# Optimization experiments

Hardware: AMD Instinct MI355X
Metric: run time of the kernel (lower is better)

Reference implementation:

```python
import jax, jax.numpy as jnp
import numpy as np

IN_DIM = 784
HIDDEN = 512
STYLE = 128
BATCH = 2048
NUM_LABELS = 10


def setup_inputs() -> dict:
    key = jax.random.key(0)
    k1, k2, k3, k4 = jax.random.split(key, 4)
    x = jax.random.uniform(k1, (BATCH, IN_DIM), dtype=jnp.float32)
    m = jax.random.randint(k2, (BATCH,), 0, NUM_LABELS)
    # Embedding tables, scaled as in the torch __init__ (N(0,1)/fan)
    fc1_table = jax.random.normal(k3, (NUM_LABELS, (IN_DIM + 1) * HIDDEN), dtype=jnp.float32) / ((IN_DIM + 1) * HIDDEN)
    fc2_table = jax.random.normal(k4, (NUM_LABELS, (HIDDEN + 1) * STYLE), dtype=jnp.float32) / ((HIDDEN + 1) * STYLE)
    return {"x": x, "m": m, "fc1_table": fc1_table, "fc2_table": fc2_table}


def reference(x, m, fc1_table, fc2_table):
    B = x.shape[0]
    x = x.reshape(B, -1)  # [B, 784]
    # Per-sample weight matrices gathered by label
    fc1 = fc1_table[m].reshape(B, IN_DIM + 1, HIDDEN)   # [B, 785, H]
    fc1_w, fc1_b = fc1[:, :IN_DIM, :], fc1[:, -1, :]
    h1 = jax.nn.relu(jnp.einsum('bkj,bk->bj', fc1_w, x) + fc1_b)  # [B, H]
    fc2 = fc2_table[m].reshape(B, HIDDEN + 1, STYLE)    # [B, H+1, S]
    fc2_w, fc2_b = fc2[:, :HIDDEN, :], fc2[:, -1, :]
    h2 = jnp.einsum('bkj,bk->bj', fc2_w, h1) + fc2_b    # [B, S]
    return jax.nn.sigmoid(h2)
```

## Files before the change

kernel.cpp:

```cpp
#include <hip/hip_runtime.h>
#include <hip/hip_bf16.h>
#include <math.h>

#define BATCH      2048
#define IN_DIM     784
#define HIDDEN     512
#define STYLE      128
#define NUM_LABELS 10
#define FC1_STRIDE ((IN_DIM + 1) * HIDDEN)
#define FC2_STRIDE ((HIDDEN + 1) * STYLE)
#define KP1        832
#define TB         64
#define BK         64
#define MAX_TILES  48

#define META_NTILES 31
#define META_TILES  32
#define META_PERM   176

#define W1B_OFF  16384ULL
#define W2B_OFF  (W1B_OFF + 10ULL*HIDDEN*KP1*2)
#define H1B_OFF  (W2B_OFF + 10ULL*STYLE*HIDDEN*2)
#define BF16_NEED (H1B_OFF + (size_t)BATCH*HIDDEN*2)

#define W1_KB 26
#define W1_NB 16
#define W2_KB 16
#define W2_NB 4
#define W1_BLOCKS (W1_KB*W1_NB*NUM_LABELS)
#define W2_BLOCKS (W2_KB*W2_NB*NUM_LABELS)

typedef short short8  __attribute__((ext_vector_type(8)));
typedef float float4e __attribute__((ext_vector_type(4)));

__device__ __forceinline__ ushort f2b(float v) {
    __hip_bfloat16 h = __float2bfloat16(v);
    return *reinterpret_cast<ushort*>(&h);
}

__global__ void k_prep(const int* __restrict__ m, const float* __restrict__ fc1t,
                       const float* __restrict__ fc2t, int* __restrict__ meta,
                       ushort* __restrict__ w1b, ushort* __restrict__ w2b) {
    const int tid = threadIdx.x;
    int bid = blockIdx.x;

    __shared__ int cnt[NUM_LABELS], curs[NUM_LABELS], offs[NUM_LABELS + 1];
    __shared__ int permS[BATCH];
    __shared__ float tile[32][33];

    if (bid == 0) {
        if (tid < NUM_LABELS) { cnt[tid] = 0; curs[tid] = 0; }
        __syncthreads();
        for (int b = tid; b < BATCH; b += 256) atomicAdd(&cnt[m[b]], 1);
        __syncthreads();
        if (tid == 0) {
            int off = 0;
            for (int L = 0; L < NUM_LABELS; ++L) { offs[L] = off; off += cnt[L]; }
            offs[NUM_LABELS] = off;
        }
        __syncthreads();
        for (int b = tid; b < BATCH; b += 256) {
            int L = m[b];
            int r = atomicAdd(&curs[L], 1);
            permS[offs[L] + r] = b;
        }
        __syncthreads();
        for (int i = tid; i < BATCH; i += 256) meta[META_PERM + i] = permS[i];
        if (tid == 0) {
            int idx = 0;
            for (int L = 0; L < NUM_LABELS; ++L) {
                int c = cnt[L], off = offs[L];
                for (int t = 0; t < c; t += TB) {
                    meta[META_TILES + idx * 3 + 0] = L;
                    meta[META_TILES + idx * 3 + 1] = off + t;
                    meta[META_TILES + idx * 3 + 2] = min(TB, c - t);
                    ++idx;
                }
            }
            meta[META_NTILES] = idx;
        }
        return;
    }

    bid -= 1;
    const float* src; ushort* dst; int Kvalid, Kpad, N, kb, nb, L; size_t srcL, dstL;
    if (bid < W1_BLOCKS) {
        kb = bid % W1_KB; nb = (bid / W1_KB) % W1_NB; L = bid / (W1_KB * W1_NB);
        src = fc1t; dst = w1b; Kvalid = IN_DIM; Kpad = KP1; N = HIDDEN;
        srcL = FC1_STRIDE; dstL = (size_t)HIDDEN * KP1;
    } else {
        bid -= W1_BLOCKS;
        kb = bid % W2_KB; nb = (bid / W2_KB) % W2_NB; L = bid / (W2_KB * W2_NB);
        src = fc2t; dst = w2b; Kvalid = HIDDEN; Kpad = HIDDEN; N = STYLE;
        srcL = FC2_STRIDE; dstL = (size_t)STYLE * HIDDEN;
    }
    const int tx = tid & 31, ty = tid >> 5;
    const int k0 = kb * 32, n0 = nb * 32;
    for (int r = ty; r < 32; r += 8) {
        int k = k0 + r;
        tile[r][tx] = (k < Kvalid) ? src[(size_t)L * srcL + (size_t)k * N + n0 + tx] : 0.f;
    }
    __syncthreads();
    for (int r = ty; r < 32; r += 8) {
        int n = n0 + r;
        dst[(size_t)L * dstL + (size_t)n * Kpad + k0 + tx] = f2b(tile[tx][r]);
    }
}

__launch_bounds__(256)
__global__ void k_fc1m(const float* __restrict__ x, const ushort* __restrict__ w1b,
                       const float* __restrict__ fc1t, const int* __restrict__ meta,
                       ushort* __restrict__ h1b) {
    const int t = blockIdx.x;
    if (t >= meta[META_NTILES]) return;
    const int L      = meta[META_TILES + 3 * t + 0];
    const int pstart = meta[META_TILES + 3 * t + 1];
    const int nrows  = meta[META_TILES + 3 * t + 2];
    const int col0   = blockIdx.y * 64;
    const ushort* __restrict__ W = w1b + (size_t)L * HIDDEN * KP1 + (size_t)col0 * KP1;

    __shared__ int rows[TB];
    __shared__ __align__(16) ushort As[2][64][72];
    __shared__ __align__(16) ushort Bs[2][64][72];

    const int tid = threadIdx.x;
    if (tid < TB) rows[tid] = (tid < nrows) ? meta[META_PERM + pstart + tid] : -1;
    __syncthreads();

    const int sr = tid >> 2, sc = tid & 3;
    const int lane = tid & 63, wv = tid >> 6;
    const int qd = lane >> 4, ln16 = lane & 15;

    const int arow = rows[sr];
    const float* __restrict__ xr = x + (size_t)(arow < 0 ? 0 : arow) * IN_DIM;
    const uint4* __restrict__ bgp = (const uint4*)(W + (size_t)sr * KP1);

    float4e acc[4] = {};
    float4 a0, a1, a2, a3;
    uint4 b0, b1;

    {
        const int ka = sc * 16;
        a0 = make_float4(0.f,0.f,0.f,0.f); a1 = a0; a2 = a0; a3 = a0;
        if (arow >= 0) {
            if (ka      < IN_DIM) a0 = *(const float4*)(xr + ka);
            if (ka + 4  < IN_DIM) a1 = *(const float4*)(xr + ka + 4);
            if (ka + 8  < IN_DIM) a2 = *(const float4*)(xr + ka + 8);
            if (ka + 12 < IN_DIM) a3 = *(const float4*)(xr + ka + 12);
        }
        b0 = bgp[sc * 2 + 0];
        b1 = bgp[sc * 2 + 1];
        ushort av[16];
        av[0]=f2b(a0.x); av[1]=f2b(a0.y); av[2]=f2b(a0.z); av[3]=f2b(a0.w);
        av[4]=f2b(a1.x); av[5]=f2b(a1.y); av[6]=f2b(a1.z); av[7]=f2b(a1.w);
        av[8]=f2b(a2.x); av[9]=f2b(a2.y); av[10]=f2b(a2.z); av[11]=f2b(a2.w);
        av[12]=f2b(a3.x); av[13]=f2b(a3.y); av[14]=f2b(a3.z); av[15]=f2b(a3.w);
        *(uint4*)&As[0][sr][sc * 16 + 0] = *(const uint4*)&av[0];
        *(uint4*)&As[0][sr][sc * 16 + 8] = *(const uint4*)&av[8];
        *(uint4*)&Bs[0][sr][sc * 16 + 0] = b0;
        *(uint4*)&Bs[0][sr][sc * 16 + 8] = b1;
    }
    {
        const int ka = BK + sc * 16;
        a0 = make_float4(0.f,0.f,0.f,0.f); a1 = a0; a2 = a0; a3 = a0;
        if (arow >= 0) {
            if (ka      < IN_DIM) a0 = *(const float4*)(xr + ka);
            if (ka + 4  < IN_DIM) a1 = *(const float4*)(xr + ka + 4);
            if (ka + 8  < IN_DIM) a2 = *(const float4*)(xr + ka + 8);
            if (ka + 12 < IN_DIM) a3 = *(const float4*)(xr + ka + 12);
        }
        b0 = bgp[(BK >> 3) + sc * 2 + 0];
        b1 = bgp[(BK >> 3) + sc * 2 + 1];
    }

    int p = 0;
    for (int k0 = 0; k0 < KP1; k0 += BK) {
        __syncthreads();
        if (k0 + BK < KP1) {
            ushort av[16];
            av[0]=f2b(a0.x); av[1]=f2b(a0.y); av[2]=f2b(a0.z); av[3]=f2b(a0.w);
            av[4]=f2b(a1.x); av[5]=f2b(a1.y); av[6]=f2b(a1.z); av[7]=f2b(a1.w);
            av[8]=f2b(a2.x); av[9]=f2b(a2.y); av[10]=f2b(a2.z); av[11]=f2b(a2.w);
            av[12]=f2b(a3.x); av[13]=f2b(a3.y); av[14]=f2b(a3.z); av[15]=f2b(a3.w);
            *(uint4*)&As[1-p][sr][sc * 16 + 0] = *(const uint4*)&av[0];
            *(uint4*)&As[1-p][sr][sc * 16 + 8] = *(const uint4*)&av[8];
            *(uint4*)&Bs[1-p][sr][sc * 16 + 0] = b0;
            *(uint4*)&Bs[1-p][sr][sc * 16 + 8] = b1;
        }
        if (k0 + 2*BK < KP1) {
            const int ka = k0 + 2*BK + sc * 16;
            a0 = make_float4(0.f,0.f,0.f,0.f); a1 = a0; a2 = a0; a3 = a0;
            if (arow >= 0) {
                if (ka      < IN_DIM) a0 = *(const float4*)(xr + ka);
                if (ka + 4  < IN_DIM) a1 = *(const float4*)(xr + ka + 4);
                if (ka + 8  < IN_DIM) a2 = *(const float4*)(xr + ka + 8);
                if (ka + 12 < IN_DIM) a3 = *(const float4*)(xr + ka + 12);
            }
            b0 = bgp[((k0 + 2*BK) >> 3) + sc * 2 + 0];
            b1 = bgp[((k0 + 2*BK) >> 3) + sc * 2 + 1];
        }
#pragma unroll
        for (int s = 0; s < 2; ++s) {
            short8 af = *(const short8*)&As[p][wv * 16 + ln16][s * 32 + qd * 8];
#pragma unroll
            for (int nt = 0; nt < 4; ++nt) {
                short8 bf = *(const short8*)&Bs[p][nt * 16 + ln16][s * 32 + qd * 8];
                acc[nt] = __builtin_amdgcn_mfma_f32_16x16x32_bf16(af, bf, acc[nt], 0, 0, 0);
            }
        }
        p ^= 1;
    }

    const float* __restrict__ bias = fc1t + (size_t)L * FC1_STRIDE + (size_t)IN_DIM * HIDDEN + col0;
#pragma unroll
    for (int nt = 0; nt < 4; ++nt) {
        const int c = nt * 16 + ln16;
        const float bs = bias[c];
#pragma unroll
        for (int i = 0; i < 4; ++i) {
            const int r = wv * 16 + qd * 4 + i;
            if (r < nrows)
                h1b[(size_t)(pstart + r) * HIDDEN + col0 + c] = f2b(fmaxf(acc[nt][i] + bs, 0.f));
        }
    }
}

__launch_bounds__(256)
__global__ void k_fc2m(const ushort* __restrict__ h1b, const ushort* __restrict__ w2b,
                       const float* __restrict__ fc2t, const int* __restrict__ meta,
                       float* __restrict__ out) {
    const int t = blockIdx.x;
    if (t >= meta[META_NTILES]) return;
    const int L      = meta[META_TILES + 3 * t + 0];
    const int pstart = meta[META_TILES + 3 * t + 1];
    const int nrows  = meta[META_TILES + 3 * t + 2];
    const int col0   = blockIdx.y * 64;
    const ushort* __restrict__ W = w2b + (size_t)L * STYLE * HIDDEN + (size_t)col0 * HIDDEN;

    __shared__ int rows[TB];
    __shared__ __align__(16) ushort As[2][64][72];
    __shared__ __align__(16) ushort Bs[2][64][72];

    const int tid = threadIdx.x;
    if (tid < TB) rows[tid] = (tid < nrows) ? meta[META_PERM + pstart + tid] : -1;
    __syncthreads();

    const int sr = tid >> 2, sc = tid & 3;
    const int lane = tid & 63, wv = tid >> 6;
    const int qd = lane >> 4, ln16 = lane & 15;

    const bool aval = (sr < nrows);
    const uint4* __restrict__ agp = (const uint4*)(h1b + (size_t)(pstart + (aval ? sr : 0)) * HIDDEN);
    const uint4* __restrict__ bgp = (const uint4*)(W + (size_t)sr * HIDDEN);

    float4e acc[4] = {};
    uint4 a0, a1, b0, b1;

    a0 = make_uint4(0u,0u,0u,0u); a1 = a0;
    if (aval) { a0 = agp[sc * 2 + 0]; a1 = agp[sc * 2 + 1]; }
    b0 = bgp[sc * 2 + 0];
    b1 = bgp[sc * 2 + 1];
    *(uint4*)&As[0][sr][sc * 16 + 0] = a0;
    *(uint4*)&As[0][sr][sc * 16 + 8] = a1;
    *(uint4*)&Bs[0][sr][sc * 16 + 0] = b0;
    *(uint4*)&Bs[0][sr][sc * 16 + 8] = b1;
    {
        const int base = (BK >> 3) + sc * 2;
        a0 = make_uint4(0u,0u,0u,0u); a1 = a0;
        if (aval) { a0 = agp[base]; a1 = agp[base + 1]; }
        b0 = bgp[base];
        b1 = bgp[base + 1];
    }

    int p = 0;
    for (int k0 = 0; k0 < HIDDEN; k0 += BK) {
        __syncthreads();
        if (k0 + BK < HIDDEN) {
            *(uint4*)&As[1-p][sr][sc * 16 + 0] = a0;
            *(uint4*)&As[1-p][sr][sc * 16 + 8] = a1;
            *(uint4*)&Bs[1-p][sr][sc * 16 + 0] = b0;
            *(uint4*)&Bs[1-p][sr][sc * 16 + 8] = b1;
        }
        if (k0 + 2*BK < HIDDEN) {
            const int base = ((k0 + 2*BK) >> 3) + sc * 2;
            a0 = make_uint4(0u,0u,0u,0u); a1 = a0;
            if (aval) { a0 = agp[base]; a1 = agp[base + 1]; }
            b0 = bgp[base];
            b1 = bgp[base + 1];
        }
#pragma unroll
        for (int s = 0; s < 2; ++s) {
            short8 af = *(const short8*)&As[p][wv * 16 + ln16][s * 32 + qd * 8];
#pragma unroll
            for (int nt = 0; nt < 4; ++nt) {
                short8 bf = *(const short8*)&Bs[p][nt * 16 + ln16][s * 32 + qd * 8];
                acc[nt] = __builtin_amdgcn_mfma_f32_16x16x32_bf16(af, bf, acc[nt], 0, 0, 0);
            }
        }
        p ^= 1;
    }

    const float* __restrict__ bias = fc2t + (size_t)L * FC2_STRIDE + (size_t)HIDDEN * STYLE + col0;
#pragma unroll
    for (int nt = 0; nt < 4; ++nt) {
        const int c = nt * 16 + ln16;
        const float bs = bias[c];
#pragma unroll
        for (int i = 0; i < 4; ++i) {
            const int r = wv * 16 + qd * 4 + i;
            if (r < nrows) {
                const int orow = rows[r];
                out[(size_t)orow * STYLE + col0 + c] = 1.f / (1.f + __expf(-(acc[nt][i] + bs)));
            }
        }
    }
}

__launch_bounds__(256)
__global__ void k_naive(const float* __restrict__ x, const int* __restrict__ m,
                        const float* __restrict__ fc1t, const float* __restrict__ fc2t,
                        float* __restrict__ out) {
    __shared__ float xs[IN_DIM];
    __shared__ float h1[HIDDEN];
    const int b = blockIdx.x, tid = threadIdx.x, L = m[b];
    for (int k = tid; k < IN_DIM; k += 256) xs[k] = x[(size_t)b * IN_DIM + k];
    __syncthreads();
    const float* __restrict__ W1 = fc1t + (size_t)L * FC1_STRIDE;
    for (int j = tid; j < HIDDEN; j += 256) {
        float acc = W1[(size_t)IN_DIM * HIDDEN + j];
        for (int k = 0; k < IN_DIM; ++k) acc = fmaf(xs[k], W1[(size_t)k * HIDDEN + j], acc);
        h1[j] = fmaxf(acc, 0.f);
    }
    __syncthreads();
    const float* __restrict__ W2 = fc2t + (size_t)L * FC2_STRIDE;
    for (int j = tid; j < STYLE; j += 256) {
        float acc = W2[(size_t)HIDDEN * STYLE + j];
        for (int k = 0; k < HIDDEN; ++k) acc = fmaf(h1[k], W2[(size_t)k * STYLE + j], acc);
        out[(size_t)b * STYLE + j] = 1.f / (1.f + __expf(-acc));
    }
}

extern "C" void kernel_launch(void* const* d_in, const int* in_sizes, int n_in,
                              void* d_out, int out_size, void* d_ws, size_t ws_size,
                              hipStream_t stream) {
    const float* x    = (const float*)d_in[0];
    const int*   m    = (const int*)d_in[1];
    const float* fc1t = (const float*)d_in[2];
    const float* fc2t = (const float*)d_in[3];
    float* out = (float*)d_out;

    if (ws_size >= BF16_NEED) {
        int*    meta = (int*)d_ws;
        ushort* w1b  = (ushort*)((char*)d_ws + W1B_OFF);
        ushort* w2b  = (ushort*)((char*)d_ws + W2B_OFF);
        ushort* h1b  = (ushort*)((char*)d_ws + H1B_OFF);

        k_prep<<<1 + W1_BLOCKS + W2_BLOCKS, 256, 0, stream>>>(m, fc1t, fc2t, meta, w1b, w2b);
        k_fc1m<<<dim3(MAX_TILES, HIDDEN / 64), 256, 0, stream>>>(x, w1b, fc1t, meta, h1b);
        k_fc2m<<<dim3(MAX_TILES, STYLE / 64), 256, 0, stream>>>(h1b, w2b, fc2t, meta, out);
    } else {
        k_naive<<<BATCH, 256, 0, stream>>>(x, m, fc1t, fc2t, out);
    }
}
```

Baseline: 101.7 us.

## Fuse weight transpose and bf16 cast into GEMM loads; ballot-based label sort

Removes the separate prep pass that transposed and converted every per-label weight table to bf16 in workspace. The GEMM kernels now read fp32 weights straight from the tables with strided per-thread loads, converting to bf16 before the shared-memory store. The label bucketing moves into a single-block kernel that counts and ranks with wave ballots and popcounts instead of shared atomics. This saves a full read and write of the weight tables plus one launch, but the strided scalar weight loads are less coalesced and each tile re-converts weights redundantly.

```diff
diff --git a/kernel.cpp b/kernel.cpp
--- a/kernel.cpp
+++ b/kernel.cpp
@@ -18,17 +18,8 @@
 #define META_TILES  32
 #define META_PERM   176
 
-#define W1B_OFF  16384ULL
-#define W2B_OFF  (W1B_OFF + 10ULL*HIDDEN*KP1*2)
-#define H1B_OFF  (W2B_OFF + 10ULL*STYLE*HIDDEN*2)
-#define BF16_NEED (H1B_OFF + (size_t)BATCH*HIDDEN*2)
-
-#define W1_KB 26
-#define W1_NB 16
-#define W2_KB 16
-#define W2_NB 4
-#define W1_BLOCKS (W1_KB*W1_NB*NUM_LABELS)
-#define W2_BLOCKS (W2_KB*W2_NB*NUM_LABELS)
+#define H1B_OFF  16384ULL
+#define WS_NEED  (H1B_OFF + (size_t)BATCH*HIDDEN*2)
 
 typedef short short8  __attribute__((ext_vector_type(8)));
 typedef float float4e __attribute__((ext_vector_type(4)));
@@ -38,86 +29,71 @@
     return *reinterpret_cast<ushort*>(&h);
 }
 
-__global__ void k_prep(const int* __restrict__ m, const float* __restrict__ fc1t,
-                       const float* __restrict__ fc2t, int* __restrict__ meta,
-                       ushort* __restrict__ w1b, ushort* __restrict__ w2b) {
+__global__ void k_meta(const int* __restrict__ m, int* __restrict__ meta) {
     const int tid = threadIdx.x;
-    int bid = blockIdx.x;
-
-    __shared__ int cnt[NUM_LABELS], curs[NUM_LABELS], offs[NUM_LABELS + 1];
-    __shared__ int permS[BATCH];
-    __shared__ float tile[32][33];
-
-    if (bid == 0) {
-        if (tid < NUM_LABELS) { cnt[tid] = 0; curs[tid] = 0; }
-        __syncthreads();
-        for (int b = tid; b < BATCH; b += 256) atomicAdd(&cnt[m[b]], 1);
-        __syncthreads();
-        if (tid == 0) {
-            int off = 0;
-            for (int L = 0; L < NUM_LABELS; ++L) { offs[L] = off; off += cnt[L]; }
-            offs[NUM_LABELS] = off;
-        }
-        __syncthreads();
-        for (int b = tid; b < BATCH; b += 256) {
-            int L = m[b];
-            int r = atomicAdd(&curs[L], 1);
-            permS[offs[L] + r] = b;
-        }
-        __syncthreads();
-        for (int i = tid; i < BATCH; i += 256) meta[META_PERM + i] = permS[i];
-        if (tid == 0) {
-            int idx = 0;
-            for (int L = 0; L < NUM_LABELS; ++L) {
-                int c = cnt[L], off = offs[L];
-                for (int t = 0; t < c; t += TB) {
-                    meta[META_TILES + idx * 3 + 0] = L;
-                    meta[META_TILES + idx * 3 + 1] = off + t;
-                    meta[META_TILES + idx * 3 + 2] = min(TB, c - t);
-                    ++idx;
-                }
-            }
-            meta[META_NTILES] = idx;
-        }
-        return;
-    }
-
-    bid -= 1;
-    const float* src; ushort* dst; int Kvalid, Kpad, N, kb, nb, L; size_t srcL, dstL;
-    if (bid < W1_BLOCKS) {
-        kb = bid % W1_KB; nb = (bid / W1_KB) % W1_NB; L = bid / (W1_KB * W1_NB);
-        src = fc1t; dst = w1b; Kvalid = IN_DIM; Kpad = KP1; N = HIDDEN;
-        srcL = FC1_STRIDE; dstL = (size_t)HIDDEN * KP1;
-    } else {
-        bid -= W1_BLOCKS;
-        kb = bid % W2_KB; nb = (bid / W2_KB) % W2_NB; L = bid / (W2_KB * W2_NB);
-        src = fc2t; dst = w2b; Kvalid = HIDDEN; Kpad = HIDDEN; N = STYLE;
-        srcL = FC2_STRIDE; dstL = (size_t)STYLE * HIDDEN;
-    }
-    const int tx = tid & 31, ty = tid >> 5;
-    const int k0 = kb * 32, n0 = nb * 32;
-    for (int r = ty; r < 32; r += 8) {
-        int k = k0 + r;
-        tile[r][tx] = (k < Kvalid) ? src[(size_t)L * srcL + (size_t)k * N + n0 + tx] : 0.f;
-    }
-    __syncthreads();
-    for (int r = ty; r < 32; r += 8) {
-        int n = n0 + r;
-        dst[(size_t)L * dstL + (size_t)n * Kpad + k0 + tx] = f2b(tile[tx][r]);
+    const int lane = tid & 63, wv = tid >> 6;
+
+    __shared__ int chunkCnt[32][NUM_LABELS];
+    __shared__ int chunkPre[32][NUM_LABELS];
+    __shared__ int labCnt[NUM_LABELS];
+    __shared__ int labOff[NUM_LABELS + 1];
+
+    for (int c = wv; c < 32; c += 4) {
+        int L = m[c * 64 + lane];
+#pragma unroll
+        for (int L0 = 0; L0 < NUM_LABELS; ++L0) {
+            unsigned long long mk = __ballot(L == L0);
+            if (lane == L0) chunkCnt[c][L0] = __popcll(mk);
+        }
+    }
+    __syncthreads();
+    if (tid < NUM_LABELS) {
+        int run = 0;
+        for (int c = 0; c < 32; ++c) { chunkPre[c][tid] = run; run += chunkCnt[c][tid]; }
+        labCnt[tid] = run;
+    }
+    __syncthreads();
+    if (tid == 0) {
+        int off = 0;
+        for (int L = 0; L < NUM_LABELS; ++L) { labOff[L] = off; off += labCnt[L]; }
+        labOff[NUM_LABELS] = off;
+        int idx = 0;
+        for (int L = 0; L < NUM_LABELS; ++L) {
+            int c = labCnt[L], o = labOff[L];
+            for (int t = 0; t < c; t += TB) {
+                meta[META_TILES + idx * 3 + 0] = L;
+                meta[META_TILES + idx * 3 + 1] = o + t;
+                meta[META_TILES + idx * 3 + 2] = min(TB, c - t);
+                ++idx;
+            }
+        }
+        meta[META_NTILES] = idx;
+    }
+    __syncthreads();
+    for (int c = wv; c < 32; c += 4) {
+        int b = c * 64 + lane;
+        int L = m[b];
+#pragma unroll
+        for (int L0 = 0; L0 < NUM_LABELS; ++L0) {
+            unsigned long long mk = __ballot(L == L0);
+            if (L == L0) {
+                int r = __popcll(mk & ((1ull << lane) - 1ull));
+                meta[META_PERM + labOff[L0] + chunkPre[c][L0] + r] = b;
+            }
+        }
     }
 }
 
 __launch_bounds__(256)
-__global__ void k_fc1m(const float* __restrict__ x, const ushort* __restrict__ w1b,
-                       const float* __restrict__ fc1t, const int* __restrict__ meta,
-                       ushort* __restrict__ h1b) {
+__global__ void k_fc1c(const float* __restrict__ x, const float* __restrict__ fc1t,
+                       const int* __restrict__ meta, ushort* __restrict__ h1b) {
     const int t = blockIdx.x;
     if (t >= meta[META_NTILES]) return;
     const int L      = meta[META_TILES + 3 * t + 0];
     const int pstart = meta[META_TILES + 3 * t + 1];
     const int nrows  = meta[META_TILES + 3 * t + 2];
     const int col0   = blockIdx.y * 64;
-    const ushort* __restrict__ W = w1b + (size_t)L * HIDDEN * KP1 + (size_t)col0 * KP1;
+    const float* __restrict__ Wf = fc1t + (size_t)L * FC1_STRIDE;
 
     __shared__ int rows[TB];
     __shared__ __align__(16) ushort As[2][64][72];
@@ -132,45 +108,55 @@
     const int qd = lane >> 4, ln16 = lane & 15;
 
     const int arow = rows[sr];
-    const float* __restrict__ xr = x + (size_t)(arow < 0 ? 0 : arow) * IN_DIM;
-    const uint4* __restrict__ bgp = (const uint4*)(W + (size_t)sr * KP1);
+    const bool aval = (arow >= 0);
+    const float* __restrict__ xr = x + (size_t)(aval ? arow : 0) * IN_DIM;
+    const float* __restrict__ wcol = Wf + col0 + sr;
 
     float4e acc[4] = {};
     float4 a0, a1, a2, a3;
-    uint4 b0, b1;
+    float bl[16];
 
     {
         const int ka = sc * 16;
         a0 = make_float4(0.f,0.f,0.f,0.f); a1 = a0; a2 = a0; a3 = a0;
-        if (arow >= 0) {
+        if (aval) {
             if (ka      < IN_DIM) a0 = *(const float4*)(xr + ka);
             if (ka + 4  < IN_DIM) a1 = *(const float4*)(xr + ka + 4);
             if (ka + 8  < IN_DIM) a2 = *(const float4*)(xr + ka + 8);
             if (ka + 12 < IN_DIM) a3 = *(const float4*)(xr + ka + 12);
         }
-        b0 = bgp[sc * 2 + 0];
-        b1 = bgp[sc * 2 + 1];
+#pragma unroll
+        for (int j = 0; j < 16; ++j) {
+            int kk = sc * 16 + j;
+            bl[j] = (kk < IN_DIM) ? wcol[(size_t)kk * HIDDEN] : 0.f;
+        }
         ushort av[16];
         av[0]=f2b(a0.x); av[1]=f2b(a0.y); av[2]=f2b(a0.z); av[3]=f2b(a0.w);
         av[4]=f2b(a1.x); av[5]=f2b(a1.y); av[6]=f2b(a1.z); av[7]=f2b(a1.w);
         av[8]=f2b(a2.x); av[9]=f2b(a2.y); av[10]=f2b(a2.z); av[11]=f2b(a2.w);
         av[12]=f2b(a3.x); av[13]=f2b(a3.y); av[14]=f2b(a3.z); av[15]=f2b(a3.w);
+        ushort bv[16];
+#pragma unroll
+        for (int j = 0; j < 16; ++j) bv[j] = f2b(bl[j]);
         *(uint4*)&As[0][sr][sc * 16 + 0] = *(const uint4*)&av[0];
         *(uint4*)&As[0][sr][sc * 16 + 8] = *(const uint4*)&av[8];
-        *(uint4*)&Bs[0][sr][sc * 16 + 0] = b0;
-        *(uint4*)&Bs[0][sr][sc * 16 + 8] = b1;
+        *(uint4*)&Bs[0][sr][sc * 16 + 0] = *(const uint4*)&bv[0];
+        *(uint4*)&Bs[0][sr][sc * 16 + 8] = *(const uint4*)&bv[8];
     }
     {
         const int ka = BK + sc * 16;
         a0 = make_float4(0.f,0.f,0.f,0.f); a1 = a0; a2 = a0; a3 = a0;
-        if (arow >= 0) {
+        if (aval) {
             if (ka      < IN_DIM) a0 = *(const float4*)(xr + ka);
             if (ka + 4  < IN_DIM) a1 = *(const float4*)(xr + ka + 4);
             if (ka + 8  < IN_DIM) a2 = *(const float4*)(xr + ka + 8);
             if (ka + 12 < IN_DIM) a3 = *(const float4*)(xr + ka + 12);
         }
-        b0 = bgp[(BK >> 3) + sc * 2 + 0];
-        b1 = bgp[(BK >> 3) + sc * 2 + 1];
+#pragma unroll
+        for (int j = 0; j < 16; ++j) {
+            int kk = BK + sc * 16 + j;
+            bl[j] = (kk < IN_DIM) ? wcol[(size_t)kk * HIDDEN] : 0.f;
+        }
     }
 
     int p = 0;
@@ -182,22 +168,28 @@
             av[4]=f2b(a1.x); av[5]=f2b(a1.y); av[6]=f2b(a1.z); av[7]=f2b(a1.w);
             av[8]=f2b(a2.x); av[9]=f2b(a2.y); av[10]=f2b(a2.z); av[11]=f2b(a2.w);
             av[12]=f2b(a3.x); av[13]=f2b(a3.y); av[14]=f2b(a3.z); av[15]=f2b(a3.w);
+            ushort bv[16];
+#pragma unroll
+            for (int j = 0; j < 16; ++j) bv[j] = f2b(bl[j]);
             *(uint4*)&As[1-p][sr][sc * 16 + 0] = *(const uint4*)&av[0];
             *(uint4*)&As[1-p][sr][sc * 16 + 8] = *(const uint4*)&av[8];
-            *(uint4*)&Bs[1-p][sr][sc * 16 + 0] = b0;
-            *(uint4*)&Bs[1-p][sr][sc * 16 + 8] = b1;
+            *(uint4*)&Bs[1-p][sr][sc * 16 + 0] = *(const uint4*)&bv[0];
+            *(uint4*)&Bs[1-p][sr][sc * 16 + 8] = *(const uint4*)&bv[8];
         }
         if (k0 + 2*BK < KP1) {
             const int ka = k0 + 2*BK + sc * 16;
             a0 = make_float4(0.f,0.f,0.f,0.f); a1 = a0; a2 = a0; a3 = a0;
-            if (arow >= 0) {
+            if (aval) {
                 if (ka      < IN_DIM) a0 = *(const float4*)(xr + ka);
                 if (ka + 4  < IN_DIM) a1 = *(const float4*)(xr + ka + 4);
                 if (ka + 8  < IN_DIM) a2 = *(const float4*)(xr + ka + 8);
                 if (ka + 12 < IN_DIM) a3 = *(const float4*)(xr + ka + 12);
             }
-            b0 = bgp[((k0 + 2*BK) >> 3) + sc * 2 + 0];
-            b1 = bgp[((k0 + 2*BK) >> 3) + sc * 2 + 1];
+#pragma unroll
+            for (int j = 0; j < 16; ++j) {
+                int kk = k0 + 2*BK + sc * 16 + j;
+                bl[j] = (kk < IN_DIM) ? wcol[(size_t)kk * HIDDEN] : 0.f;
+            }
         }
 #pragma unroll
         for (int s = 0; s < 2; ++s) {
@@ -226,16 +218,15 @@
 }
 
 __launch_bounds__(256)
-__global__ void k_fc2m(const ushort* __restrict__ h1b, const ushort* __restrict__ w2b,
-                       const float* __restrict__ fc2t, const int* __restrict__ meta,
-                       float* __restrict__ out) {
+__global__ void k_fc2c(const ushort* __restrict__ h1b, const float* __restrict__ fc2t,
+                       const int* __restrict__ meta, float* __restrict__ out) {
     const int t = blockIdx.x;
     if (t >= meta[META_NTILES]) return;
     const int L      = meta[META_TILES + 3 * t + 0];
     const int pstart = meta[META_TILES + 3 * t + 1];
     const int nrows  = meta[META_TILES + 3 * t + 2];
     const int col0   = blockIdx.y * 64;
-    const ushort* __restrict__ W = w2b + (size_t)L * STYLE * HIDDEN + (size_t)col0 * HIDDEN;
+    const float* __restrict__ Wf = fc2t + (size_t)L * FC2_STRIDE;
 
     __shared__ int rows[TB];
     __shared__ __align__(16) ushort As[2][64][72];
@@ -251,42 +242,51 @@
 
     const bool aval = (sr < nrows);
     const uint4* __restrict__ agp = (const uint4*)(h1b + (size_t)(pstart + (aval ? sr : 0)) * HIDDEN);
-    const uint4* __restrict__ bgp = (const uint4*)(W + (size_t)sr * HIDDEN);
+    const float* __restrict__ wcol = Wf + col0 + sr;
 
     float4e acc[4] = {};
-    uint4 a0, a1, b0, b1;
+    uint4 a0, a1;
+    float bl[16];
 
     a0 = make_uint4(0u,0u,0u,0u); a1 = a0;
     if (aval) { a0 = agp[sc * 2 + 0]; a1 = agp[sc * 2 + 1]; }
-    b0 = bgp[sc * 2 + 0];
-    b1 = bgp[sc * 2 + 1];
-    *(uint4*)&As[0][sr][sc * 16 + 0] = a0;
-    *(uint4*)&As[0][sr][sc * 16 + 8] = a1;
-    *(uint4*)&Bs[0][sr][sc * 16 + 0] = b0;
-    *(uint4*)&Bs[0][sr][sc * 16 + 8] = b1;
+#pragma unroll
+    for (int j = 0; j < 16; ++j) bl[j] = wcol[(size_t)(sc * 16 + j) * STYLE];
+    {
+        ushort bv[16];
+#pragma unroll
+        for (int j = 0; j < 16; ++j) bv[j] = f2b(bl[j]);
+        *(uint4*)&As[0][sr][sc * 16 + 0] = a0;
+        *(uint4*)&As[0][sr][sc * 16 + 8] = a1;
+        *(uint4*)&Bs[0][sr][sc * 16 + 0] = *(const uint4*)&bv[0];
+        *(uint4*)&Bs[0][sr][sc * 16 + 8] = *(const uint4*)&bv[8];
+    }
     {
         const int base = (BK >> 3) + sc * 2;
         a0 = make_uint4(0u,0u,0u,0u); a1 = a0;
         if (aval) { a0 = agp[base]; a1 = agp[base + 1]; }
-        b0 = bgp[base];
-        b1 = bgp[base + 1];
+#pragma unroll
+        for (int j = 0; j < 16; ++j) bl[j] = wcol[(size_t)(BK + sc * 16 + j) * STYLE];
     }
 
     int p = 0;
     for (int k0 = 0; k0 < HIDDEN; k0 += BK) {
         __syncthreads();
         if (k0 + BK < HIDDEN) {
+            ushort bv[16];
+#pragma unroll
+            for (int j = 0; j < 16; ++j) bv[j] = f2b(bl[j]);
             *(uint4*)&As[1-p][sr][sc * 16 + 0] = a0;
             *(uint4*)&As[1-p][sr][sc * 16 + 8] = a1;
-            *(uint4*)&Bs[1-p][sr][sc * 16 + 0] = b0;
-            *(uint4*)&Bs[1-p][sr][sc * 16 + 8] = b1;
+            *(uint4*)&Bs[1-p][sr][sc * 16 + 0] = *(const uint4*)&bv[0];
+            *(uint4*)&Bs[1-p][sr][sc * 16 + 8] = *(const uint4*)&bv[8];
         }
         if (k0 + 2*BK < HIDDEN) {
             const int base = ((k0 + 2*BK) >> 3) + sc * 2;
             a0 = make_uint4(0u,0u,0u,0u); a1 = a0;
             if (aval) { a0 = agp[base]; a1 = agp[base + 1]; }
-            b0 = bgp[base];
-            b1 = bgp[base + 1];
+#pragma unroll
+            for (int j = 0; j < 16; ++j) bl[j] = wcol[(size_t)(k0 + 2*BK + sc * 16 + j) * STYLE];
         }
 #pragma unroll
         for (int s = 0; s < 2; ++s) {
@@ -349,15 +349,13 @@
     const float* fc2t = (const float*)d_in[3];
     float* out = (float*)d_out;
 
-    if (ws_size >= BF16_NEED) {
+    if (ws_size >= WS_NEED) {
         int*    meta = (int*)d_ws;
-        ushort* w1b  = (ushort*)((char*)d_ws + W1B_OFF);
-        ushort* w2b  = (ushort*)((char*)d_ws + W2B_OFF);
         ushort* h1b  = (ushort*)((char*)d_ws + H1B_OFF);
 
-        k_prep<<<1 + W1_BLOCKS + W2_BLOCKS, 256, 0, stream>>>(m, fc1t, fc2t, meta, w1b, w2b);
-        k_fc1m<<<dim3(MAX_TILES, HIDDEN / 64), 256, 0, stream>>>(x, w1b, fc1t, meta, h1b);
-        k_fc2m<<<dim3(MAX_TILES, STYLE / 64), 256, 0, stream>>>(h1b, w2b, fc2t, meta, out);
+        k_meta<<<1, 256, 0, stream>>>(m, meta);
+        k_fc1c<<<dim3(MAX_TILES, HIDDEN / 64), 256, 0, stream>>>(x, fc1t, meta, h1b);
+        k_fc2c<<<dim3(MAX_TILES, STYLE / 64), 256, 0, stream>>>(h1b, fc2t, meta, out);
     } else {
         k_naive<<<BATCH, 256, 0, stream>>>(x, m, fc1t, fc2t, out);
     }
```

New measurement: 126.8 us. 24.7% more time.

## Halve GEMM column tiles to double grid blocks; ballot-based deterministic label sort

Applied to the files above, without the earlier changes.

Shrinks the output column tile in both grouped GEMM kernels from 64 to 32. This doubles the number of blocks, giving more parallelism across the many CUs, at the cost of reloading the activation tile twice as often and issuing fewer MFMAs per block. Also replaces the shared-memory atomic counting sort of labels with a wave-ballot, per-chunk prefix scheme that writes the permutation directly and shares LDS through a union. The new sort is deterministic, but its scan runs serially over 32 chunks on a few threads.

```diff
diff --git a/kernel.cpp b/kernel.cpp
--- a/kernel.cpp
+++ b/kernel.cpp
@@ -21,7 +21,7 @@
 #define W1B_OFF  16384ULL
 #define W2B_OFF  (W1B_OFF + 10ULL*HIDDEN*KP1*2)
 #define H1B_OFF  (W2B_OFF + 10ULL*STYLE*HIDDEN*2)
-#define BF16_NEED (H1B_OFF + (size_t)BATCH*HIDDEN*2)
+#define WS_NEED  (H1B_OFF + (size_t)BATCH*HIDDEN*2)
 
 #define W1_KB 26
 #define W1_NB 16
@@ -43,41 +43,62 @@
                        ushort* __restrict__ w1b, ushort* __restrict__ w2b) {
     const int tid = threadIdx.x;
     int bid = blockIdx.x;
-
-    __shared__ int cnt[NUM_LABELS], curs[NUM_LABELS], offs[NUM_LABELS + 1];
-    __shared__ int permS[BATCH];
-    __shared__ float tile[32][33];
+    const int lane = tid & 63, wv = tid >> 6;
+
+    __shared__ union __align__(16) {
+        float tile[32][33];
+        struct {
+            int chunkCnt[32][NUM_LABELS];
+            int chunkPre[32][NUM_LABELS];
+            int labCnt[NUM_LABELS];
+            int labOff[NUM_LABELS + 1];
+        } mt;
+    } sm;
 
     if (bid == 0) {
-        if (tid < NUM_LABELS) { cnt[tid] = 0; curs[tid] = 0; }
-        __syncthreads();
-        for (int b = tid; b < BATCH; b += 256) atomicAdd(&cnt[m[b]], 1);
+        for (int c = wv; c < 32; c += 4) {
+            int L = m[c * 64 + lane];
+#pragma unroll
+            for (int L0 = 0; L0 < NUM_LABELS; ++L0) {
+                unsigned long long mk = __ballot(L == L0);
+                if (lane == L0) sm.mt.chunkCnt[c][L0] = __popcll(mk);
+            }
+        }
+        __syncthreads();
+        if (tid < NUM_LABELS) {
+            int run = 0;
+            for (int c = 0; c < 32; ++c) { sm.mt.chunkPre[c][tid] = run; run += sm.mt.chunkCnt[c][tid]; }
+            sm.mt.labCnt[tid] = run;
+        }
         __syncthreads();
         if (tid == 0) {
             int off = 0;
-            for (int L = 0; L < NUM_LABELS; ++L) { offs[L] = off; off += cnt[L]; }
-            offs[NUM_LABELS] = off;
-        }
-        __syncthreads();
-        for (int b = tid; b < BATCH; b += 256) {
-            int L = m[b];
-            int r = atomicAdd(&curs[L], 1);
-            permS[offs[L] + r] = b;
-        }
-        __syncthreads();
-        for (int i = tid; i < BATCH; i += 256) meta[META_PERM + i] = permS[i];
-        if (tid == 0) {
+            for (int L = 0; L < NUM_LABELS; ++L) { sm.mt.labOff[L] = off; off += sm.mt.labCnt[L]; }
+            sm.mt.labOff[NUM_LABELS] = off;
             int idx = 0;
             for (int L = 0; L < NUM_LABELS; ++L) {
-                int c = cnt[L], off = offs[L];
+                int c = sm.mt.labCnt[L], o = sm.mt.labOff[L];
                 for (int t = 0; t < c; t += TB) {
                     meta[META_TILES + idx * 3 + 0] = L;
-                    meta[META_TILES + idx * 3 + 1] = off + t;
+                    meta[META_TILES + idx * 3 + 1] = o + t;
                     meta[META_TILES + idx * 3 + 2] = min(TB, c - t);
                     ++idx;
                 }
             }
             meta[META_NTILES] = idx;
+        }
+        __syncthreads();
+        for (int c = wv; c < 32; c += 4) {
+            int b = c * 64 + lane;
+            int L = m[b];
+#pragma unroll
+            for (int L0 = 0; L0 < NUM_LABELS; ++L0) {
+                unsigned long long mk = __ballot(L == L0);
+                if (L == L0) {
+                    int r = __popcll(mk & ((1ull << lane) - 1ull));
+                    meta[META_PERM + sm.mt.labOff[L0] + sm.mt.chunkPre[c][L0] + r] = b;
+                }
+            }
         }
         return;
     }
@@ -98,12 +119,12 @@
     const int k0 = kb * 32, n0 = nb * 32;
     for (int r = ty; r < 32; r += 8) {
         int k = k0 + r;
-        tile[r][tx] = (k < Kvalid) ? src[(size_t)L * srcL + (size_t)k * N + n0 + tx] : 0.f;
+        sm.tile[r][tx] = (k < Kvalid) ? src[(size_t)L * srcL + (size_t)k * N + n0 + tx] : 0.f;
     }
     __syncthreads();
     for (int r = ty; r < 32; r += 8) {
         int n = n0 + r;
-        dst[(size_t)L * dstL + (size_t)n * Kpad + k0 + tx] = f2b(tile[tx][r]);
+        dst[(size_t)L * dstL + (size_t)n * Kpad + k0 + tx] = f2b(sm.tile[tx][r]);
     }
 }
 
@@ -116,40 +137,41 @@
     const int L      = meta[META_TILES + 3 * t + 0];
     const int pstart = meta[META_TILES + 3 * t + 1];
     const int nrows  = meta[META_TILES + 3 * t + 2];
-    const int col0   = blockIdx.y * 64;
+    const int col0   = blockIdx.y * 32;
     const ushort* __restrict__ W = w1b + (size_t)L * HIDDEN * KP1 + (size_t)col0 * KP1;
 
     __shared__ int rows[TB];
     __shared__ __align__(16) ushort As[2][64][72];
-    __shared__ __align__(16) ushort Bs[2][64][72];
+    __shared__ __align__(16) ushort Bs[2][32][72];
 
     const int tid = threadIdx.x;
     if (tid < TB) rows[tid] = (tid < nrows) ? meta[META_PERM + pstart + tid] : -1;
     __syncthreads();
 
     const int sr = tid >> 2, sc = tid & 3;
+    const int sb = tid >> 3, scb = tid & 7;
     const int lane = tid & 63, wv = tid >> 6;
     const int qd = lane >> 4, ln16 = lane & 15;
 
     const int arow = rows[sr];
-    const float* __restrict__ xr = x + (size_t)(arow < 0 ? 0 : arow) * IN_DIM;
-    const uint4* __restrict__ bgp = (const uint4*)(W + (size_t)sr * KP1);
-
-    float4e acc[4] = {};
+    const bool aval = (arow >= 0);
+    const float* __restrict__ xr = x + (size_t)(aval ? arow : 0) * IN_DIM;
+    const uint4* __restrict__ bgp = (const uint4*)(W + (size_t)sb * KP1);
+
+    float4e acc[2] = {};
     float4 a0, a1, a2, a3;
-    uint4 b0, b1;
+    uint4 b0;
 
     {
         const int ka = sc * 16;
         a0 = make_float4(0.f,0.f,0.f,0.f); a1 = a0; a2 = a0; a3 = a0;
-        if (arow >= 0) {
+        if (aval) {
             if (ka      < IN_DIM) a0 = *(const float4*)(xr + ka);
             if (ka + 4  < IN_DIM) a1 = *(const float4*)(xr + ka + 4);
             if (ka + 8  < IN_DIM) a2 = *(const float4*)(xr + ka + 8);
             if (ka + 12 < IN_DIM) a3 = *(const float4*)(xr + ka + 12);
         }
-        b0 = bgp[sc * 2 + 0];
-        b1 = bgp[sc * 2 + 1];
+        b0 = bgp[scb];
         ushort av[16];
         av[0]=f2b(a0.x); av[1]=f2b(a0.y); av[2]=f2b(a0.z); av[3]=f2b(a0.w);
         av[4]=f2b(a1.x); av[5]=f2b(a1.y); av[6]=f2b(a1.z); av[7]=f2b(a1.w);
@@ -157,20 +179,18 @@
         av[12]=f2b(a3.x); av[13]=f2b(a3.y); av[14]=f2b(a3.z); av[15]=f2b(a3.w);
         *(uint4*)&As[0][sr][sc * 16 + 0] = *(const uint4*)&av[0];
         *(uint4*)&As[0][sr][sc * 16 + 8] = *(const uint4*)&av[8];
-        *(uint4*)&Bs[0][sr][sc * 16 + 0] = b0;
-        *(uint4*)&Bs[0][sr][sc * 16 + 8] = b1;
+        *(uint4*)&Bs[0][sb][scb * 8]     = b0;
     }
     {
         const int ka = BK + sc * 16;
         a0 = make_float4(0.f,0.f,0.f,0.f); a1 = a0; a2 = a0; a3 = a0;
-        if (arow >= 0) {
+        if (aval) {
             if (ka      < IN_DIM) a0 = *(const float4*)(xr + ka);
             if (ka + 4  < IN_DIM) a1 = *(const float4*)(xr + ka + 4);
             if (ka + 8  < IN_DIM) a2 = *(const float4*)(xr + ka + 8);
             if (ka + 12 < IN_DIM) a3 = *(const float4*)(xr + ka + 12);
         }
-        b0 = bgp[(BK >> 3) + sc * 2 + 0];
-        b1 = bgp[(BK >> 3) + sc * 2 + 1];
+        b0 = bgp[(BK >> 3) + scb];
     }
 
     int p = 0;
@@ -184,26 +204,24 @@
             av[12]=f2b(a3.x); av[13]=f2b(a3.y); av[14]=f2b(a3.z); av[15]=f2b(a3.w);
             *(uint4*)&As[1-p][sr][sc * 16 + 0] = *(const uint4*)&av[0];
             *(uint4*)&As[1-p][sr][sc * 16 + 8] = *(const uint4*)&av[8];
-            *(uint4*)&Bs[1-p][sr][sc * 16 + 0] = b0;
-            *(uint4*)&Bs[1-p][sr][sc * 16 + 8] = b1;
+            *(uint4*)&Bs[1-p][sb][scb * 8]     = b0;
         }
         if (k0 + 2*BK < KP1) {
             const int ka = k0 + 2*BK + sc * 16;
             a0 = make_float4(0.f,0.f,0.f,0.f); a1 = a0; a2 = a0; a3 = a0;
-            if (arow >= 0) {
+            if (aval) {
                 if (ka      < IN_DIM) a0 = *(const float4*)(xr + ka);
                 if (ka + 4  < IN_DIM) a1 = *(const float4*)(xr + ka + 4);
                 if (ka + 8  < IN_DIM) a2 = *(const float4*)(xr + ka + 8);
                 if (ka + 12 < IN_DIM) a3 = *(const float4*)(xr + ka + 12);
             }
-            b0 = bgp[((k0 + 2*BK) >> 3) + sc * 2 + 0];
-            b1 = bgp[((k0 + 2*BK) >> 3) + sc * 2 + 1];
+            b0 = bgp[((k0 + 2*BK) >> 3) + scb];
         }
 #pragma unroll
         for (int s = 0; s < 2; ++s) {
             short8 af = *(const short8*)&As[p][wv * 16 + ln16][s * 32 + qd * 8];
 #pragma unroll
-            for (int nt = 0; nt < 4; ++nt) {
+            for (int nt = 0; nt < 2; ++nt) {
                 short8 bf = *(const short8*)&Bs[p][nt * 16 + ln16][s * 32 + qd * 8];
                 acc[nt] = __builtin_amdgcn_mfma_f32_16x16x32_bf16(af, bf, acc[nt], 0, 0, 0);
             }
@@ -213,7 +231,7 @@
 
     const float* __restrict__ bias = fc1t + (size_t)L * FC1_STRIDE + (size_t)IN_DIM * HIDDEN + col0;
 #pragma unroll
-    for (int nt = 0; nt < 4; ++nt) {
+    for (int nt = 0; nt < 2; ++nt) {
         const int c = nt * 16 + ln16;
         const float bs = bias[c];
 #pragma unroll
@@ -234,42 +252,40 @@
     const int L      = meta[META_TILES + 3 * t + 0];
     const int pstart = meta[META_TILES + 3 * t + 1];
     const int nrows  = meta[META_TILES + 3 * t + 2];
-    const int col0   = blockIdx.y * 64;
+    const int col0   = blockIdx.y * 32;
     const ushort* __restrict__ W = w2b + (size_t)L * STYLE * HIDDEN + (size_t)col0 * HIDDEN;
 
     __shared__ int rows[TB];
     __shared__ __align__(16) ushort As[2][64][72];
-    __shared__ __align__(16) ushort Bs[2][64][72];
+    __shared__ __align__(16) ushort Bs[2][32][72];
 
     const int tid = threadIdx.x;
     if (tid < TB) rows[tid] = (tid < nrows) ? meta[META_PERM + pstart + tid] : -1;
     __syncthreads();
 
     const int sr = tid >> 2, sc = tid & 3;
+    const int sb = tid >> 3, scb = tid & 7;
     const int lane = tid & 63, wv = tid >> 6;
     const int qd = lane >> 4, ln16 = lane & 15;
 
     const bool aval = (sr < nrows);
     const uint4* __restrict__ agp = (const uint4*)(h1b + (size_t)(pstart + (aval ? sr : 0)) * HIDDEN);
-    const uint4* __restrict__ bgp = (const uint4*)(W + (size_t)sr * HIDDEN);
-
-    float4e acc[4] = {};
-    uint4 a0, a1, b0, b1;
+    const uint4* __restrict__ bgp = (const uint4*)(W + (size_t)sb * HIDDEN);
+
+    float4e acc[2] = {};
+    uint4 a0, a1, b0;
 
     a0 = make_uint4(0u,0u,0u,0u); a1 = a0;
     if (aval) { a0 = agp[sc * 2 + 0]; a1 = agp[sc * 2 + 1]; }
-    b0 = bgp[sc * 2 + 0];
-    b1 = bgp[sc * 2 + 1];
+    b0 = bgp[scb];
     *(uint4*)&As[0][sr][sc * 16 + 0] = a0;
     *(uint4*)&As[0][sr][sc * 16 + 8] = a1;
-    *(uint4*)&Bs[0][sr][sc * 16 + 0] = b0;
-    *(uint4*)&Bs[0][sr][sc * 16 + 8] = b1;
+    *(uint4*)&Bs[0][sb][scb * 8]     = b0;
     {
         const int base = (BK >> 3) + sc * 2;
         a0 = make_uint4(0u,0u,0u,0u); a1 = a0;
         if (aval) { a0 = agp[base]; a1 = agp[base + 1]; }
-        b0 = bgp[base];
-        b1 = bgp[base + 1];
+        b0 = bgp[(BK >> 3) + scb];
     }
 
     int p = 0;
@@ -278,21 +294,19 @@
         if (k0 + BK < HIDDEN) {
             *(uint4*)&As[1-p][sr][sc * 16 + 0] = a0;
             *(uint4*)&As[1-p][sr][sc * 16 + 8] = a1;
-            *(uint4*)&Bs[1-p][sr][sc * 16 + 0] = b0;
-            *(uint4*)&Bs[1-p][sr][sc * 16 + 8] = b1;
+            *(uint4*)&Bs[1-p][sb][scb * 8]     = b0;
         }
         if (k0 + 2*BK < HIDDEN) {
             const int base = ((k0 + 2*BK) >> 3) + sc * 2;
             a0 = make_uint4(0u,0u,0u,0u); a1 = a0;
             if (aval) { a0 = agp[base]; a1 = agp[base + 1]; }
-            b0 = bgp[base];
-            b1 = bgp[base + 1];
+            b0 = bgp[((k0 + 2*BK) >> 3) + scb];
         }
 #pragma unroll
         for (int s = 0; s < 2; ++s) {
             short8 af = *(const short8*)&As[p][wv * 16 + ln16][s * 32 + qd * 8];
 #pragma unroll
-            for (int nt = 0; nt < 4; ++nt) {
+            for (int nt = 0; nt < 2; ++nt) {
                 short8 bf = *(const short8*)&Bs[p][nt * 16 + ln16][s * 32 + qd * 8];
                 acc[nt] = __builtin_amdgcn_mfma_f32_16x16x32_bf16(af, bf, acc[nt], 0, 0, 0);
             }
@@ -302,7 +316,7 @@
 
     const float* __restrict__ bias = fc2t + (size_t)L * FC2_STRIDE + (size_t)HIDDEN * STYLE + col0;
 #pragma unroll
-    for (int nt = 0; nt < 4; ++nt) {
+    for (int nt = 0; nt < 2; ++nt) {
         const int c = nt * 16 + ln16;
         const float bs = bias[c];
 #pragma unroll
@@ -349,15 +363,15 @@
     const float* fc2t = (const float*)d_in[3];
     float* out = (float*)d_out;
 
-    if (ws_size >= BF16_NEED) {
+    if (ws_size >= WS_NEED) {
         int*    meta = (int*)d_ws;
         ushort* w1b  = (ushort*)((char*)d_ws + W1B_OFF);
         ushort* w2b  = (ushort*)((char*)d_ws + W2B_OFF);
         ushort* h1b  = (ushort*)((char*)d_ws + H1B_OFF);
 
         k_prep<<<1 + W1_BLOCKS + W2_BLOCKS, 256, 0, stream>>>(m, fc1t, fc2t, meta, w1b, w2b);
-        k_fc1m<<<dim3(MAX_TILES, HIDDEN / 64), 256, 0, stream>>>(x, w1b, fc1t, meta, h1b);
-        k_fc2m<<<dim3(MAX_TILES, STYLE / 64), 256, 0, stream>>>(h1b, w2b, fc2t, meta, out);
+        k_fc1m<<<dim3(MAX_TILES, HIDDEN / 32), 256, 0, stream>>>(x, w1b, fc1t, meta, h1b);
+        k_fc2m<<<dim3(MAX_TILES, STYLE / 32), 256, 0, stream>>>(h1b, w2b, fc2t, meta, out);
     } else {
         k_naive<<<BATCH, 256, 0, stream>>>(x, m, fc1t, fc2t, out);
     }
```

Result: slower. 107.8 us (+6.0%).
